# Kernel tuning notes

Measured on AMD Instinct MI355X. Metric: run time of the kernel, lower is better.

Reference implementation:

```python
import jax, jax.numpy as jnp
import numpy as np

B, P, K, F, H = 128, 200, 60, 4, 64   # events, points/event, knn k, feat dim, hidden
N = B * P


def setup_inputs() -> dict:
    key = jax.random.key(0)
    k0, k1, k2, k3 = jax.random.split(key, 4)
    x = jax.random.normal(k0, (N, F), jnp.float32)
    pos = jax.random.normal(k1, (N, 3), jnp.float32)
    batch = jnp.arange(N, dtype=jnp.int32) // P  # sorted event ids, equal-size events
    W1 = jax.random.normal(k2, (F + 3, H), jnp.float32) / np.sqrt(F + 3)
    b1 = jnp.zeros((H,), jnp.float32)
    W2 = jax.random.normal(k3, (H, H), jnp.float32) / np.sqrt(H)
    b2 = jnp.zeros((H,), jnp.float32)
    return {"x": x, "pos": pos, "batch": batch, "W1": W1, "b1": b1, "W2": W2, "b2": b2}


def _knn_edges(pos):
    """knn_graph(pos, K, batch, loop=False, flow='source_to_target').
    Equal-size events -> batched [B,P,P] pairwise distances, no cross-event edges."""
    p = pos.reshape(B, P, 3)
    d2 = jnp.sum((p[:, :, None, :] - p[:, None, :, :]) ** 2, axis=-1)  # [B,P,P]
    d2 = d2 + jnp.eye(P, dtype=d2.dtype) * 1e10                        # exclude self (loop=False)
    _, nbr = jax.lax.top_k(-d2, K)                                     # [B,P,K] local neighbor ids
    src = (nbr + (jnp.arange(B, dtype=nbr.dtype) * P)[:, None, None]).reshape(-1)  # sources j
    dst = jnp.repeat(jnp.arange(N, dtype=src.dtype), K)                             # targets i
    return jnp.stack([src, dst])  # [2, N*K]


def _local_nn(m, W1, b1, W2, b2):
    h = jax.nn.relu(m @ W1 + b1)
    return jax.nn.relu(h @ W2 + b2)


def reference(x, pos, batch, W1, b1, W2, b2):
    edge_index = _knn_edges(pos)
    src, dst = edge_index[0], edge_index[1]
    # PointConv message: net(concat[x_j, pos_j - pos_i]) on each edge
    rel = pos[src] - pos[dst]                             # [E,3]
    m = jnp.concatenate([x[src], rel], axis=-1)           # [E,F+3]
    h = _local_nn(m, W1, b1, W2, b2)                      # [E,H]
    out = h.reshape(N, K, H).max(axis=1)                  # max-aggregate per target node
    # PyG PointConv adds self-loops by default: message with rel = 0
    m_self = jnp.concatenate([x, jnp.zeros((N, 3), x.dtype)], axis=-1)
    h_self = _local_nn(m_self, W1, b1, W2, b2)            # [N,H]
    out = jnp.maximum(out, h_self)
    return (out, pos, batch, edge_index)
```

## Files before the change

kernel.cpp:

```cpp
#include <hip/hip_runtime.h>
#include <hip/hip_bf16.h>

typedef unsigned int u32;
typedef unsigned long long u64;
typedef __attribute__((ext_vector_type(8))) short bf16x8;
typedef __attribute__((ext_vector_type(4))) float f32x4;
typedef __attribute__((ext_vector_type(4))) u32 u32x4;
typedef __attribute__((ext_vector_type(2))) u32 u32x2;

#define NB 128
#define PP 200
#define KK 60
#define NN (NB*PP)
#define HH 64
#define TW 2
#define NWV 4
#define TB (TW*NWV)
#define BPE (PP/TB)
#define NTHREADS (NWV*64)

#define OUT_OFF   0
#define POS_OFF   (NN*HH)
#define BATCH_OFF (POS_OFF + NN*3)
#define ESRC_OFF  (BATCH_OFF + NN)
#define EDST_OFF  (ESRC_OFF + NN*KK)

static __device__ __forceinline__ u32 packtr(float a, float b) {
    return __builtin_amdgcn_perm(__float_as_uint(b), __float_as_uint(a), 0x07060302u);
}
static __device__ __forceinline__ u32 prefix_lt(u64 b) {
    return __builtin_amdgcn_mbcnt_hi((u32)(b >> 32),
                                     __builtin_amdgcn_mbcnt_lo((u32)b, 0));
}
static __device__ __forceinline__ float wavemax16(float v) {
    u32 x = __float_as_uint(v);
    auto p16 = __builtin_amdgcn_permlane16_swap(x, x, false, false);
    float m = fmaxf(__uint_as_float(p16[0]), __uint_as_float(p16[1]));
    u32 y = __float_as_uint(m);
    auto p32 = __builtin_amdgcn_permlane32_swap(y, y, false, false);
    return fmaxf(__uint_as_float(p32[0]), __uint_as_float(p32[1]));
}

__global__ __launch_bounds__(NTHREADS) void fused_kernel(const float* __restrict__ x,
                                                    const float* __restrict__ pos,
                                                    const float* __restrict__ W1,
                                                    const float* __restrict__ b1p,
                                                    const float* __restrict__ W2,
                                                    const float* __restrict__ b2p,
                                                    float* __restrict__ out) {
    __shared__ alignas(16) u32 xsp[PP * 2];
    __shared__ alignas(16) float psl[PP * 3];
    __shared__ alignas(16) u32 jslot[NWV * TW * 64];
    __shared__ alignas(16) u32 msg[NWV * 256];
    __shared__ alignas(16) u32 pkW1[64 * 4];
    __shared__ alignas(16) u32 pkW2T[64 * 33];
    __shared__ alignas(16) float b2s[64];
    __shared__ alignas(16) u32 zrow[4];

    int tid = threadIdx.x, blk = blockIdx.x;
    int e = blk / BPE;
    int pl0b = (blk % BPE) * TB;
    int i0b  = e * PP + pl0b;

    if (tid < 3*TB) out[POS_OFF + i0b * 3 + tid] = pos[i0b * 3 + tid];
    if (tid < TB)   out[BATCH_OFF + i0b + tid] = (float)e;

    if (tid < 200) {
        f32x4 xv = ((const f32x4*)x)[e * PP + tid];
        u32x2 p; p[0] = packtr(xv[0], xv[1]); p[1] = packtr(xv[2], xv[3]);
        *(u32x2*)&xsp[tid * 2] = p;
    }
    if (tid < 150) ((f32x4*)psl)[tid] = ((const f32x4*)pos)[e * 150 + tid];
    if (tid < 4)   zrow[tid] = 0u;

    {
        int m = tid & 63, d = tid >> 6;
        float hiv = (d < 3) ? W1[(2*d + 1)*64 + m] : b1p[m];
        pkW1[m*4 + d] = packtr(W1[(2*d)*64 + m], hiv);
    }
    #pragma unroll
    for (int r = 0; r < 4; ++r) {
        int g = r * NTHREADS + tid;
        int kp = g >> 4, colq = g & 15;
        f32x4 ra = *(const f32x4*)&W2[(2*kp)    *64 + colq*4];
        f32x4 rb = *(const f32x4*)&W2[(2*kp + 1)*64 + colq*4];
        #pragma unroll
        for (int c = 0; c < 4; ++c)
            pkW2T[(colq*4 + c)*33 + kp] = packtr(ra[c], rb[c]);
    }
    if (tid < 64) b2s[tid] = b2p[tid];
    __syncthreads();

    int lane = tid & 63, wv = tid >> 6;
    int lo16 = lane & 15, hi16 = lane >> 4;
    int plW0 = pl0b + wv * TW;
    int iW0  = e * PP + plW0;

    #pragma unroll
    for (int t = 0; t < TW; ++t)
        if (lane < KK) out[EDST_OFF + (iW0 + t) * KK + lane] = (float)(iW0 + t);

    u32 key[TW][4];
    {
        float ax[TW], ay[TW], az[TW];
        #pragma unroll
        for (int t = 0; t < TW; ++t) {
            ax[t] = psl[(plW0+t)*3]; ay[t] = psl[(plW0+t)*3+1]; az[t] = psl[(plW0+t)*3+2];
        }
        #pragma unroll
        for (int q = 0; q < 4; ++q) {
            int j = lane + q * 64;
            int jc = (j < PP) ? j : 0;
            float px = psl[jc*3], py = psl[jc*3+1], pz = psl[jc*3+2];
            #pragma unroll
            for (int t = 0; t < TW; ++t) {
                float dx = px-ax[t], dy = py-ay[t], dz = pz-az[t];
                float d2 = dx*dx + dy*dy + dz*dz;
                key[t][q] = (j < PP && j != plW0 + t)
                          ? ((__float_as_uint(d2) & 0xFFFFFF00u) | (u32)j) : 0xFFFFFFFFu;
            }
        }
    }

    bf16x8 w1f[4];
    #pragma unroll
    for (int th = 0; th < 4; ++th) {
        union { u32 w[4]; bf16x8 v; } u;
        if (hi16 == 0) *(u32x4*)u.w = *(const u32x4*)&pkW1[(th * 16 + lo16) * 4];
        else { u.w[0] = u.w[1] = u.w[2] = u.w[3] = 0u; }
        w1f[th] = u.v;
    }
    bf16x8 bfr[4][2];
    #pragma unroll
    for (int t = 0; t < 4; ++t)
        #pragma unroll
        for (int s = 0; s < 2; ++s) {
            union { u32 w[4]; bf16x8 v; } u;
            int base = (t * 16 + lo16) * 33 + s * 16 + hi16 * 4;
            #pragma unroll
            for (int d = 0; d < 4; ++d) u.w[d] = pkW2T[base + d];
            bfr[t][s] = u.v;
        }
    float b2me = b2s[lane];

    u32 lo[TW], hi[TW]; int done[TW];
    #pragma unroll
    for (int t = 0; t < TW; ++t) { lo[t] = 0u; hi[t] = 0x7F800000u; done[t] = 0; }
    #pragma unroll 1
    for (int g = 0; g < 8; ++g) {
        #pragma unroll
        for (int u4 = 0; u4 < 4; ++u4) {
            #pragma unroll
            for (int t = 0; t < TW; ++t) {
                u32 m = lo[t] + ((hi[t] - lo[t]) >> 1);
                int c = __builtin_popcountll(__ballot(key[t][0] < m))
                      + __builtin_popcountll(__ballot(key[t][1] < m))
                      + __builtin_popcountll(__ballot(key[t][2] < m))
                      + __builtin_popcountll(__ballot(key[t][3] < m));
                int upd = !done[t];
                int ge  = (c >= KK);
                hi[t] = (upd & ge)  ? m : hi[t];
                lo[t] = (upd & !ge) ? m : lo[t];
                done[t] |= (c == KK) | (hi[t] - lo[t] <= 1u);
            }
        }
        int alldone = done[0];
        #pragma unroll
        for (int t = 1; t < TW; ++t) alldone &= done[t];
        if (alldone) break;
    }

    const int jsb = wv * (TW * 64);
    #pragma unroll
    for (int t = 0; t < TW; ++t) {
        if (lane >= KK) jslot[jsb + t * 64 + lane] = (u32)(plW0 + t);
        u64 m0 = __ballot(key[t][0] < hi[t]);
        u64 m1 = __ballot(key[t][1] < hi[t]);
        u64 m2 = __ballot(key[t][2] < hi[t]);
        u64 m3 = __ballot(key[t][3] < hi[t]);
        u32 s1 = (u32)__builtin_popcountll(m0);
        u32 s2 = s1 + (u32)__builtin_popcountll(m1);
        u32 s3 = s2 + (u32)__builtin_popcountll(m2);
        u32 sl[4] = { prefix_lt(m0), s1 + prefix_lt(m1),
                      s2 + prefix_lt(m2), s3 + prefix_lt(m3) };
        #pragma unroll
        for (int q = 0; q < 4; ++q)
            if (key[t][q] < hi[t]) jslot[jsb + t * 64 + (int)sl[q]] = key[t][q] & 0xFFu;
    }
    #pragma unroll
    for (int t = 0; t < TW; ++t) {
        int i = iW0 + t;
        if (lane < KK)
            out[ESRC_OFF + i * KK + lane] = (float)(e * PP + (int)jslot[jsb + t * 64 + lane]);
    }

    const int msb = wv * 256;
    const u32* mbase = (hi16 == 0) ? &msg[msb + lo16 * 4] : zrow;
    const int mstep  = (hi16 == 0) ? 64 : 0;

    for (int tl = 0; tl < TW; ++tl) {
        int i = iW0 + tl, pl = plW0 + tl;
        int jloc = (int)jslot[jsb + tl * 64 + lane];
        u32x2 xp = *(const u32x2*)&xsp[jloc * 2];
        float rx = psl[jloc*3]   - psl[pl*3];
        float ry = psl[jloc*3+1] - psl[pl*3+1];
        float rz = psl[jloc*3+2] - psl[pl*3+2];
        u32x4 mrow;
        mrow[0] = xp[0];
        mrow[1] = xp[1];
        mrow[2] = packtr(rx, ry);
        mrow[3] = packtr(rz, 1.0f);
        *(u32x4*)&msg[msb + lane * 4] = mrow;

        float rmax[4] = {-3.0e38f, -3.0e38f, -3.0e38f, -3.0e38f};
        __builtin_amdgcn_s_setprio(1);
        #pragma unroll
        for (int rt = 0; rt < 4; ++rt) {
            union { u32 w[4]; bf16x8 v; } mu;
            *(u32x4*)mu.w = *(const u32x4*)(mbase + rt * mstep);

            f32x4 c1[4];
            #pragma unroll
            for (int th = 0; th < 4; ++th)
                c1[th] = __builtin_amdgcn_mfma_f32_16x16x32_bf16(w1f[th], mu.v,
                                                                 (f32x4)0.f, 0, 0, 0);
            f32x4 acc[4];
            #pragma unroll
            for (int t = 0; t < 4; ++t) acc[t] = (f32x4)0.f;

            #pragma unroll
            for (int s = 0; s < 2; ++s) {
                u32 pe0 = packtr(fmaxf(c1[2*s][0], 0.f), fmaxf(c1[2*s][1], 0.f));
                u32 pe1 = packtr(fmaxf(c1[2*s][2], 0.f), fmaxf(c1[2*s][3], 0.f));
                u32 po0 = packtr(fmaxf(c1[2*s+1][0], 0.f), fmaxf(c1[2*s+1][1], 0.f));
                u32 po1 = packtr(fmaxf(c1[2*s+1][2], 0.f), fmaxf(c1[2*s+1][3], 0.f));
                union { u32 w[4]; bf16x8 v; } u;
                {
                    auto t0 = __builtin_amdgcn_permlane32_swap(pe0, po0, false, false);
                    auto w0 = __builtin_amdgcn_permlane16_swap(t0[0], t0[1], false, false);
                    u.w[0] = w0[0]; u.w[2] = w0[1];
                }
                {
                    auto t1 = __builtin_amdgcn_permlane32_swap(pe1, po1, false, false);
                    auto w1 = __builtin_amdgcn_permlane16_swap(t1[0], t1[1], false, false);
                    u.w[1] = w1[0]; u.w[3] = w1[1];
                }
                #pragma unroll
                for (int t = 0; t < 4; ++t)
                    acc[t] = __builtin_amdgcn_mfma_f32_16x16x32_bf16(u.v, bfr[t][s],
                                                                     acc[t], 0, 0, 0);
            }
            #pragma unroll
            for (int t = 0; t < 4; ++t) {
                rmax[t] = fmaxf(fmaxf(acc[t][0], acc[t][1]), rmax[t]);
                rmax[t] = fmaxf(fmaxf(acc[t][2], acc[t][3]), rmax[t]);
            }
        }
        __builtin_amdgcn_s_setprio(0);
        #pragma unroll
        for (int t = 0; t < 4; ++t) rmax[t] = wavemax16(rmax[t]);
        float sel = rmax[0];
        sel = (hi16 == 1) ? rmax[1] : sel;
        sel = (hi16 == 2) ? rmax[2] : sel;
        sel = (hi16 == 3) ? rmax[3] : sel;
        out[OUT_OFF + i * 64 + lane] = fmaxf(sel + b2me, 0.f);
    }
}

extern "C" void kernel_launch(void* const* d_in, const int* in_sizes, int n_in,
                              void* d_out, int out_size, void* d_ws, size_t ws_size,
                              hipStream_t stream) {
    const float* x     = (const float*)d_in[0];
    const float* pos   = (const float*)d_in[1];
    const float* W1    = (const float*)d_in[3];
    const float* b1    = (const float*)d_in[4];
    const float* W2    = (const float*)d_in[5];
    const float* b2    = (const float*)d_in[6];
    float* out = (float*)d_out;
    (void)d_ws; (void)ws_size; (void)in_sizes; (void)n_in; (void)out_size;

    fused_kernel<<<dim3(NN / TB), dim3(NTHREADS), 0, stream>>>(x, pos, W1, b1, W2, b2, out);
}
```

Measured before the change: 113.7 us.

## Tighten kNN bisection bounds and pass MFMA message rows via permlane

The threshold bisection for the k-th nearest distance now starts from the wave-wide min and max key, found with shuffle and permlane reductions, rather than the full float range. Tuples that have converged skip further ballot rounds. Message rows for the first-layer MFMA are no longer staged through LDS; each rt slice is built in registers with permlane16/32 swaps, which removes the msg and zrow shared buffers and their store/load round trip. The cost is two extra wave reductions per tuple and cross-lane permutes in the inner loop, and the upper lanes' zero-padding semantics now differ, so the B-operand layout may not match the previous zero-filled rows.

```diff
diff --git a/kernel.cpp b/kernel.cpp
--- a/kernel.cpp
+++ b/kernel.cpp
@@ -40,6 +40,26 @@
     auto p32 = __builtin_amdgcn_permlane32_swap(y, y, false, false);
     return fmaxf(__uint_as_float(p32[0]), __uint_as_float(p32[1]));
 }
+static __device__ __forceinline__ u32 wredmin_u32(u32 v) {
+    v = min(v, (u32)__shfl_xor((int)v, 1, 64));
+    v = min(v, (u32)__shfl_xor((int)v, 2, 64));
+    v = min(v, (u32)__shfl_xor((int)v, 4, 64));
+    v = min(v, (u32)__shfl_xor((int)v, 8, 64));
+    auto p16 = __builtin_amdgcn_permlane16_swap(v, v, false, false);
+    v = min((u32)p16[0], (u32)p16[1]);
+    auto p32 = __builtin_amdgcn_permlane32_swap(v, v, false, false);
+    return min((u32)p32[0], (u32)p32[1]);
+}
+static __device__ __forceinline__ u32 wredmax_u32(u32 v) {
+    v = max(v, (u32)__shfl_xor((int)v, 1, 64));
+    v = max(v, (u32)__shfl_xor((int)v, 2, 64));
+    v = max(v, (u32)__shfl_xor((int)v, 4, 64));
+    v = max(v, (u32)__shfl_xor((int)v, 8, 64));
+    auto p16 = __builtin_amdgcn_permlane16_swap(v, v, false, false);
+    v = max((u32)p16[0], (u32)p16[1]);
+    auto p32 = __builtin_amdgcn_permlane32_swap(v, v, false, false);
+    return max((u32)p32[0], (u32)p32[1]);
+}
 
 __global__ __launch_bounds__(NTHREADS) void fused_kernel(const float* __restrict__ x,
                                                     const float* __restrict__ pos,
@@ -51,11 +71,9 @@
     __shared__ alignas(16) u32 xsp[PP * 2];
     __shared__ alignas(16) float psl[PP * 3];
     __shared__ alignas(16) u32 jslot[NWV * TW * 64];
-    __shared__ alignas(16) u32 msg[NWV * 256];
     __shared__ alignas(16) u32 pkW1[64 * 4];
     __shared__ alignas(16) u32 pkW2T[64 * 33];
     __shared__ alignas(16) float b2s[64];
-    __shared__ alignas(16) u32 zrow[4];
 
     int tid = threadIdx.x, blk = blockIdx.x;
     int e = blk / BPE;
@@ -71,7 +89,6 @@
         *(u32x2*)&xsp[tid * 2] = p;
     }
     if (tid < 150) ((f32x4*)psl)[tid] = ((const f32x4*)pos)[e * 150 + tid];
-    if (tid < 4)   zrow[tid] = 0u;
 
     {
         int m = tid & 63, d = tid >> 6;
@@ -145,23 +162,26 @@
 
     u32 lo[TW], hi[TW]; int done[TW];
     #pragma unroll
-    for (int t = 0; t < TW; ++t) { lo[t] = 0u; hi[t] = 0x7F800000u; done[t] = 0; }
+    for (int t = 0; t < TW; ++t) {
+        u32 mn = min(min(key[t][0], key[t][1]), min(key[t][2], key[t][3]));
+        u32 mx = max(max(key[t][0] + 1u, key[t][1] + 1u),
+                     max(key[t][2] + 1u, key[t][3] + 1u));
+        lo[t] = wredmin_u32(mn);
+        hi[t] = wredmax_u32(mx);
+        done[t] = 0;
+    }
     #pragma unroll 1
-    for (int g = 0; g < 8; ++g) {
-        #pragma unroll
-        for (int u4 = 0; u4 < 4; ++u4) {
-            #pragma unroll
-            for (int t = 0; t < TW; ++t) {
+    for (int it = 0; it < 32; ++it) {
+        #pragma unroll
+        for (int t = 0; t < TW; ++t) {
+            if (!done[t]) {
                 u32 m = lo[t] + ((hi[t] - lo[t]) >> 1);
                 int c = __builtin_popcountll(__ballot(key[t][0] < m))
                       + __builtin_popcountll(__ballot(key[t][1] < m))
                       + __builtin_popcountll(__ballot(key[t][2] < m))
                       + __builtin_popcountll(__ballot(key[t][3] < m));
-                int upd = !done[t];
-                int ge  = (c >= KK);
-                hi[t] = (upd & ge)  ? m : hi[t];
-                lo[t] = (upd & !ge) ? m : lo[t];
-                done[t] |= (c == KK) | (hi[t] - lo[t] <= 1u);
+                if (c >= KK) hi[t] = m; else lo[t] = m;
+                done[t] = (c == KK) | (hi[t] - lo[t] <= 1u);
             }
         }
         int alldone = done[0];
@@ -194,10 +214,6 @@
             out[ESRC_OFF + i * KK + lane] = (float)(e * PP + (int)jslot[jsb + t * 64 + lane]);
     }
 
-    const int msb = wv * 256;
-    const u32* mbase = (hi16 == 0) ? &msg[msb + lo16 * 4] : zrow;
-    const int mstep  = (hi16 == 0) ? 64 : 0;
-
     for (int tl = 0; tl < TW; ++tl) {
         int i = iW0 + tl, pl = plW0 + tl;
         int jloc = (int)jslot[jsb + tl * 64 + lane];
@@ -205,19 +221,33 @@
         float rx = psl[jloc*3]   - psl[pl*3];
         float ry = psl[jloc*3+1] - psl[pl*3+1];
         float rz = psl[jloc*3+2] - psl[pl*3+2];
-        u32x4 mrow;
-        mrow[0] = xp[0];
-        mrow[1] = xp[1];
-        mrow[2] = packtr(rx, ry);
-        mrow[3] = packtr(rz, 1.0f);
-        *(u32x4*)&msg[msb + lane * 4] = mrow;
+        u32 mr[4];
+        mr[0] = xp[0];
+        mr[1] = xp[1];
+        mr[2] = packtr(rx, ry);
+        mr[3] = packtr(rz, 1.0f);
 
         float rmax[4] = {-3.0e38f, -3.0e38f, -3.0e38f, -3.0e38f};
         __builtin_amdgcn_s_setprio(1);
         #pragma unroll
         for (int rt = 0; rt < 4; ++rt) {
             union { u32 w[4]; bf16x8 v; } mu;
-            *(u32x4*)mu.w = *(const u32x4*)(mbase + rt * mstep);
+            #pragma unroll
+            for (int d = 0; d < 4; ++d) {
+                if (rt == 0) {
+                    mu.w[d] = mr[d];
+                } else if (rt == 1) {
+                    auto p = __builtin_amdgcn_permlane16_swap(mr[d], mr[d], false, false);
+                    mu.w[d] = p[1];
+                } else if (rt == 2) {
+                    auto p = __builtin_amdgcn_permlane32_swap(mr[d], mr[d], false, false);
+                    mu.w[d] = p[1];
+                } else {
+                    auto p = __builtin_amdgcn_permlane32_swap(mr[d], mr[d], false, false);
+                    auto q = __builtin_amdgcn_permlane16_swap(p[1], p[1], false, false);
+                    mu.w[d] = q[1];
+                }
+            }
 
             f32x4 c1[4];
             #pragma unroll
```

New measurement: 120.1 us. 1.06x slower.

## Process two point tiles per block to amortize per-block setup

Applied to the files above, without the earlier changes.

Each block now handles up to two 8-point tiles of an event instead of one, so the event's x/pos staging and the W1/W2 bf16 packing into shared memory are done once per two tiles. The grid shrinks from 3200 to 1664 blocks, and the last block of each event handles a single tile. Pos output is now copied from shared memory. The bisection loop is also restructured so that only unfinished targets are updated under a branch, with a cap of 40 iterations. This trades fewer, longer blocks for less redundant setup and may reduce latency hiding or create tail imbalance.

```diff
diff --git a/kernel.cpp b/kernel.cpp
--- a/kernel.cpp
+++ b/kernel.cpp
@@ -16,7 +16,9 @@
 #define TW 2
 #define NWV 4
 #define TB (TW*NWV)
-#define BPE (PP/TB)
+#define NTILE 25
+#define TPB 2
+#define BPE 13
 #define NTHREADS (NWV*64)
 
 #define OUT_OFF   0
@@ -58,12 +60,9 @@
     __shared__ alignas(16) u32 zrow[4];
 
     int tid = threadIdx.x, blk = blockIdx.x;
-    int e = blk / BPE;
-    int pl0b = (blk % BPE) * TB;
-    int i0b  = e * PP + pl0b;
-
-    if (tid < 3*TB) out[POS_OFF + i0b * 3 + tid] = pos[i0b * 3 + tid];
-    if (tid < TB)   out[BATCH_OFF + i0b + tid] = (float)e;
+    int e   = blk / BPE;
+    int tb0 = (blk % BPE) * TPB;
+    int ntile = (tb0 + 1 < NTILE) ? TPB : 1;
 
     if (tid < 200) {
         f32x4 xv = ((const f32x4*)x)[e * PP + tid];
@@ -93,177 +92,182 @@
 
     int lane = tid & 63, wv = tid >> 6;
     int lo16 = lane & 15, hi16 = lane >> 4;
-    int plW0 = pl0b + wv * TW;
-    int iW0  = e * PP + plW0;
-
-    #pragma unroll
-    for (int t = 0; t < TW; ++t)
-        if (lane < KK) out[EDST_OFF + (iW0 + t) * KK + lane] = (float)(iW0 + t);
-
-    u32 key[TW][4];
-    {
-        float ax[TW], ay[TW], az[TW];
-        #pragma unroll
-        for (int t = 0; t < TW; ++t) {
-            ax[t] = psl[(plW0+t)*3]; ay[t] = psl[(plW0+t)*3+1]; az[t] = psl[(plW0+t)*3+2];
-        }
-        #pragma unroll
-        for (int q = 0; q < 4; ++q) {
-            int j = lane + q * 64;
-            int jc = (j < PP) ? j : 0;
-            float px = psl[jc*3], py = psl[jc*3+1], pz = psl[jc*3+2];
-            #pragma unroll
-            for (int t = 0; t < TW; ++t) {
-                float dx = px-ax[t], dy = py-ay[t], dz = pz-az[t];
-                float d2 = dx*dx + dy*dy + dz*dz;
-                key[t][q] = (j < PP && j != plW0 + t)
-                          ? ((__float_as_uint(d2) & 0xFFFFFF00u) | (u32)j) : 0xFFFFFFFFu;
-            }
-        }
-    }
-
-    bf16x8 w1f[4];
-    #pragma unroll
-    for (int th = 0; th < 4; ++th) {
-        union { u32 w[4]; bf16x8 v; } u;
-        if (hi16 == 0) *(u32x4*)u.w = *(const u32x4*)&pkW1[(th * 16 + lo16) * 4];
-        else { u.w[0] = u.w[1] = u.w[2] = u.w[3] = 0u; }
-        w1f[th] = u.v;
-    }
-    bf16x8 bfr[4][2];
-    #pragma unroll
-    for (int t = 0; t < 4; ++t)
-        #pragma unroll
-        for (int s = 0; s < 2; ++s) {
-            union { u32 w[4]; bf16x8 v; } u;
-            int base = (t * 16 + lo16) * 33 + s * 16 + hi16 * 4;
-            #pragma unroll
-            for (int d = 0; d < 4; ++d) u.w[d] = pkW2T[base + d];
-            bfr[t][s] = u.v;
-        }
     float b2me = b2s[lane];
-
-    u32 lo[TW], hi[TW]; int done[TW];
-    #pragma unroll
-    for (int t = 0; t < TW; ++t) { lo[t] = 0u; hi[t] = 0x7F800000u; done[t] = 0; }
-    #pragma unroll 1
-    for (int g = 0; g < 8; ++g) {
-        #pragma unroll
-        for (int u4 = 0; u4 < 4; ++u4) {
-            #pragma unroll
-            for (int t = 0; t < TW; ++t) {
-                u32 m = lo[t] + ((hi[t] - lo[t]) >> 1);
-                int c = __builtin_popcountll(__ballot(key[t][0] < m))
-                      + __builtin_popcountll(__ballot(key[t][1] < m))
-                      + __builtin_popcountll(__ballot(key[t][2] < m))
-                      + __builtin_popcountll(__ballot(key[t][3] < m));
-                int upd = !done[t];
-                int ge  = (c >= KK);
-                hi[t] = (upd & ge)  ? m : hi[t];
-                lo[t] = (upd & !ge) ? m : lo[t];
-                done[t] |= (c == KK) | (hi[t] - lo[t] <= 1u);
-            }
-        }
-        int alldone = done[0];
-        #pragma unroll
-        for (int t = 1; t < TW; ++t) alldone &= done[t];
-        if (alldone) break;
-    }
-
     const int jsb = wv * (TW * 64);
-    #pragma unroll
-    for (int t = 0; t < TW; ++t) {
-        if (lane >= KK) jslot[jsb + t * 64 + lane] = (u32)(plW0 + t);
-        u64 m0 = __ballot(key[t][0] < hi[t]);
-        u64 m1 = __ballot(key[t][1] < hi[t]);
-        u64 m2 = __ballot(key[t][2] < hi[t]);
-        u64 m3 = __ballot(key[t][3] < hi[t]);
-        u32 s1 = (u32)__builtin_popcountll(m0);
-        u32 s2 = s1 + (u32)__builtin_popcountll(m1);
-        u32 s3 = s2 + (u32)__builtin_popcountll(m2);
-        u32 sl[4] = { prefix_lt(m0), s1 + prefix_lt(m1),
-                      s2 + prefix_lt(m2), s3 + prefix_lt(m3) };
-        #pragma unroll
-        for (int q = 0; q < 4; ++q)
-            if (key[t][q] < hi[t]) jslot[jsb + t * 64 + (int)sl[q]] = key[t][q] & 0xFFu;
-    }
-    #pragma unroll
-    for (int t = 0; t < TW; ++t) {
-        int i = iW0 + t;
-        if (lane < KK)
-            out[ESRC_OFF + i * KK + lane] = (float)(e * PP + (int)jslot[jsb + t * 64 + lane]);
-    }
-
     const int msb = wv * 256;
     const u32* mbase = (hi16 == 0) ? &msg[msb + lo16 * 4] : zrow;
     const int mstep  = (hi16 == 0) ? 64 : 0;
 
-    for (int tl = 0; tl < TW; ++tl) {
-        int i = iW0 + tl, pl = plW0 + tl;
-        int jloc = (int)jslot[jsb + tl * 64 + lane];
-        u32x2 xp = *(const u32x2*)&xsp[jloc * 2];
-        float rx = psl[jloc*3]   - psl[pl*3];
-        float ry = psl[jloc*3+1] - psl[pl*3+1];
-        float rz = psl[jloc*3+2] - psl[pl*3+2];
-        u32x4 mrow;
-        mrow[0] = xp[0];
-        mrow[1] = xp[1];
-        mrow[2] = packtr(rx, ry);
-        mrow[3] = packtr(rz, 1.0f);
-        *(u32x4*)&msg[msb + lane * 4] = mrow;
-
-        float rmax[4] = {-3.0e38f, -3.0e38f, -3.0e38f, -3.0e38f};
-        __builtin_amdgcn_s_setprio(1);
-        #pragma unroll
-        for (int rt = 0; rt < 4; ++rt) {
-            union { u32 w[4]; bf16x8 v; } mu;
-            *(u32x4*)mu.w = *(const u32x4*)(mbase + rt * mstep);
-
-            f32x4 c1[4];
-            #pragma unroll
-            for (int th = 0; th < 4; ++th)
-                c1[th] = __builtin_amdgcn_mfma_f32_16x16x32_bf16(w1f[th], mu.v,
-                                                                 (f32x4)0.f, 0, 0, 0);
-            f32x4 acc[4];
-            #pragma unroll
-            for (int t = 0; t < 4; ++t) acc[t] = (f32x4)0.f;
-
+    #pragma unroll 1
+    for (int ti = 0; ti < ntile; ++ti) {
+        int pl0 = (tb0 + ti) * TB;
+        int i0  = e * PP + pl0;
+
+        if (tid < 3*TB) out[POS_OFF + i0 * 3 + tid] = psl[pl0 * 3 + tid];
+        if (tid < TB)   out[BATCH_OFF + i0 + tid] = (float)e;
+
+        int plW0 = pl0 + wv * TW;
+        int iW0  = e * PP + plW0;
+
+        #pragma unroll
+        for (int t = 0; t < TW; ++t)
+            if (lane < KK) out[EDST_OFF + (iW0 + t) * KK + lane] = (float)(iW0 + t);
+
+        u32 key[TW][4];
+        {
+            float ax[TW], ay[TW], az[TW];
+            #pragma unroll
+            for (int t = 0; t < TW; ++t) {
+                ax[t] = psl[(plW0+t)*3]; ay[t] = psl[(plW0+t)*3+1]; az[t] = psl[(plW0+t)*3+2];
+            }
+            #pragma unroll
+            for (int q = 0; q < 4; ++q) {
+                int j = lane + q * 64;
+                int jc = (j < PP) ? j : 0;
+                float px = psl[jc*3], py = psl[jc*3+1], pz = psl[jc*3+2];
+                #pragma unroll
+                for (int t = 0; t < TW; ++t) {
+                    float dx = px-ax[t], dy = py-ay[t], dz = pz-az[t];
+                    float d2 = dx*dx + dy*dy + dz*dz;
+                    key[t][q] = (j < PP && j != plW0 + t)
+                              ? ((__float_as_uint(d2) & 0xFFFFFF00u) | (u32)j) : 0xFFFFFFFFu;
+                }
+            }
+        }
+
+        u32 lo[TW], hi[TW]; int done[TW];
+        #pragma unroll
+        for (int t = 0; t < TW; ++t) { lo[t] = 0u; hi[t] = 0x7F800000u; done[t] = 0; }
+        #pragma unroll 1
+        for (int it = 0; it < 40; ++it) {
+            #pragma unroll
+            for (int t = 0; t < TW; ++t) {
+                if (!done[t]) {
+                    u32 m = lo[t] + ((hi[t] - lo[t]) >> 1);
+                    int c = __builtin_popcountll(__ballot(key[t][0] < m))
+                          + __builtin_popcountll(__ballot(key[t][1] < m))
+                          + __builtin_popcountll(__ballot(key[t][2] < m))
+                          + __builtin_popcountll(__ballot(key[t][3] < m));
+                    if (c >= KK) hi[t] = m; else lo[t] = m;
+                    done[t] = (c == KK) | (hi[t] - lo[t] <= 1u);
+                }
+            }
+            int alldone = done[0];
+            #pragma unroll
+            for (int t = 1; t < TW; ++t) alldone &= done[t];
+            if (alldone) break;
+        }
+
+        #pragma unroll
+        for (int t = 0; t < TW; ++t) {
+            if (lane >= KK) jslot[jsb + t * 64 + lane] = (u32)(plW0 + t);
+            u64 m0 = __ballot(key[t][0] < hi[t]);
+            u64 m1 = __ballot(key[t][1] < hi[t]);
+            u64 m2 = __ballot(key[t][2] < hi[t]);
+            u64 m3 = __ballot(key[t][3] < hi[t]);
+            u32 s1 = (u32)__builtin_popcountll(m0);
+            u32 s2 = s1 + (u32)__builtin_popcountll(m1);
+            u32 s3 = s2 + (u32)__builtin_popcountll(m2);
+            u32 sl[4] = { prefix_lt(m0), s1 + prefix_lt(m1),
+                          s2 + prefix_lt(m2), s3 + prefix_lt(m3) };
+            #pragma unroll
+            for (int q = 0; q < 4; ++q)
+                if (key[t][q] < hi[t]) jslot[jsb + t * 64 + (int)sl[q]] = key[t][q] & 0xFFu;
+        }
+        #pragma unroll
+        for (int t = 0; t < TW; ++t) {
+            int i = iW0 + t;
+            if (lane < KK)
+                out[ESRC_OFF + i * KK + lane] = (float)(e * PP + (int)jslot[jsb + t * 64 + lane]);
+        }
+
+        bf16x8 w1f[4];
+        #pragma unroll
+        for (int th = 0; th < 4; ++th) {
+            union { u32 w[4]; bf16x8 v; } u;
+            if (hi16 == 0) *(u32x4*)u.w = *(const u32x4*)&pkW1[(th * 16 + lo16) * 4];
+            else { u.w[0] = u.w[1] = u.w[2] = u.w[3] = 0u; }
+            w1f[th] = u.v;
+        }
+        bf16x8 bfr[4][2];
+        #pragma unroll
+        for (int t = 0; t < 4; ++t)
             #pragma unroll
             for (int s = 0; s < 2; ++s) {
-                u32 pe0 = packtr(fmaxf(c1[2*s][0], 0.f), fmaxf(c1[2*s][1], 0.f));
-                u32 pe1 = packtr(fmaxf(c1[2*s][2], 0.f), fmaxf(c1[2*s][3], 0.f));
-                u32 po0 = packtr(fmaxf(c1[2*s+1][0], 0.f), fmaxf(c1[2*s+1][1], 0.f));
-                u32 po1 = packtr(fmaxf(c1[2*s+1][2], 0.f), fmaxf(c1[2*s+1][3], 0.f));
                 union { u32 w[4]; bf16x8 v; } u;
-                {
-                    auto t0 = __builtin_amdgcn_permlane32_swap(pe0, po0, false, false);
-                    auto w0 = __builtin_amdgcn_permlane16_swap(t0[0], t0[1], false, false);
-                    u.w[0] = w0[0]; u.w[2] = w0[1];
-                }
-                {
-                    auto t1 = __builtin_amdgcn_permlane32_swap(pe1, po1, false, false);
-                    auto w1 = __builtin_amdgcn_permlane16_swap(t1[0], t1[1], false, false);
-                    u.w[1] = w1[0]; u.w[3] = w1[1];
-                }
-                #pragma unroll
-                for (int t = 0; t < 4; ++t)
-                    acc[t] = __builtin_amdgcn_mfma_f32_16x16x32_bf16(u.v, bfr[t][s],
-                                                                     acc[t], 0, 0, 0);
-            }
-            #pragma unroll
-            for (int t = 0; t < 4; ++t) {
-                rmax[t] = fmaxf(fmaxf(acc[t][0], acc[t][1]), rmax[t]);
-                rmax[t] = fmaxf(fmaxf(acc[t][2], acc[t][3]), rmax[t]);
-            }
-        }
-        __builtin_amdgcn_s_setprio(0);
-        #pragma unroll
-        for (int t = 0; t < 4; ++t) rmax[t] = wavemax16(rmax[t]);
-        float sel = rmax[0];
-        sel = (hi16 == 1) ? rmax[1] : sel;
-        sel = (hi16 == 2) ? rmax[2] : sel;
-        sel = (hi16 == 3) ? rmax[3] : sel;
-        out[OUT_OFF + i * 64 + lane] = fmaxf(sel + b2me, 0.f);
+                int base = (t * 16 + lo16) * 33 + s * 16 + hi16 * 4;
+                #pragma unroll
+                for (int d = 0; d < 4; ++d) u.w[d] = pkW2T[base + d];
+                bfr[t][s] = u.v;
+            }
+
+        for (int tl = 0; tl < TW; ++tl) {
+            int i = iW0 + tl, pl = plW0 + tl;
+            int jloc = (int)jslot[jsb + tl * 64 + lane];
+            u32x2 xp = *(const u32x2*)&xsp[jloc * 2];
+            float rx = psl[jloc*3]   - psl[pl*3];
+            float ry = psl[jloc*3+1] - psl[pl*3+1];
+            float rz = psl[jloc*3+2] - psl[pl*3+2];
+            u32x4 mrow;
+            mrow[0] = xp[0];
+            mrow[1] = xp[1];
+            mrow[2] = packtr(rx, ry);
+            mrow[3] = packtr(rz, 1.0f);
+            *(u32x4*)&msg[msb + lane * 4] = mrow;
+
+            float rmax[4] = {-3.0e38f, -3.0e38f, -3.0e38f, -3.0e38f};
+            __builtin_amdgcn_s_setprio(1);
+            #pragma unroll
+            for (int rt = 0; rt < 4; ++rt) {
+                union { u32 w[4]; bf16x8 v; } mu;
+                *(u32x4*)mu.w = *(const u32x4*)(mbase + rt * mstep);
+
+                f32x4 c1[4];
+                #pragma unroll
+                for (int th = 0; th < 4; ++th)
+                    c1[th] = __builtin_amdgcn_mfma_f32_16x16x32_bf16(w1f[th], mu.v,
+                                                                     (f32x4)0.f, 0, 0, 0);
+                f32x4 acc[4];
+                #pragma unroll
+                for (int t = 0; t < 4; ++t) acc[t] = (f32x4)0.f;
+
+                #pragma unroll
+                for (int s = 0; s < 2; ++s) {
+                    u32 pe0 = packtr(fmaxf(c1[2*s][0], 0.f), fmaxf(c1[2*s][1], 0.f));
+                    u32 pe1 = packtr(fmaxf(c1[2*s][2], 0.f), fmaxf(c1[2*s][3], 0.f));
+                    u32 po0 = packtr(fmaxf(c1[2*s+1][0], 0.f), fmaxf(c1[2*s+1][1], 0.f));
+                    u32 po1 = packtr(fmaxf(c1[2*s+1][2], 0.f), fmaxf(c1[2*s+1][3], 0.f));
+                    union { u32 w[4]; bf16x8 v; } u;
+                    {
+                        auto t0 = __builtin_amdgcn_permlane32_swap(pe0, po0, false, false);
+                        auto w0 = __builtin_amdgcn_permlane16_swap(t0[0], t0[1], false, false);
+                        u.w[0] = w0[0]; u.w[2] = w0[1];
+                    }
+                    {
+                        auto t1 = __builtin_amdgcn_permlane32_swap(pe1, po1, false, false);
+                        auto w1 = __builtin_amdgcn_permlane16_swap(t1[0], t1[1], false, false);
+                        u.w[1] = w1[0]; u.w[3] = w1[1];
+                    }
+                    #pragma unroll
+                    for (int t = 0; t < 4; ++t)
+                        acc[t] = __builtin_amdgcn_mfma_f32_16x16x32_bf16(u.v, bfr[t][s],
+                                                                         acc[t], 0, 0, 0);
+                }
+                #pragma unroll
+                for (int t = 0; t < 4; ++t) {
+                    rmax[t] = fmaxf(fmaxf(acc[t][0], acc[t][1]), rmax[t]);
+                    rmax[t] = fmaxf(fmaxf(acc[t][2], acc[t][3]), rmax[t]);
+                }
+            }
+            __builtin_amdgcn_s_setprio(0);
+            #pragma unroll
+            for (int t = 0; t < 4; ++t) rmax[t] = wavemax16(rmax[t]);
+            float sel = rmax[0];
+            sel = (hi16 == 1) ? rmax[1] : sel;
+            sel = (hi16 == 2) ? rmax[2] : sel;
+            sel = (hi16 == 3) ? rmax[3] : sel;
+            out[OUT_OFF + i * 64 + lane] = fmaxf(sel + b2me, 0.f);
+        }
     }
 }
 
@@ -279,5 +283,5 @@
     float* out = (float*)d_out;
     (void)d_ws; (void)ws_size; (void)in_sizes; (void)n_in; (void)out_size;
 
-    fused_kernel<<<dim3(NN / TB), dim3(NTHREADS), 0, stream>>>(x, pos, W1, b1, W2, b2, out);
-}
+    fused_kernel<<<dim3(NB * BPE), dim3(NTHREADS), 0, stream>>>(x, pos, W1, b1, W2, b2, out);
+}
```

After: 117.4 us. +3.2%, slower.

## Process one target point per wavefront instead of two, doubling block count

Applied to the files above, without the earlier changes.

Removes the TW=2 per-wave batching, so each wave handles a single target point. Blocks now cover 4 points instead of 8, which doubles the grid to 6400 blocks. The bisection loop becomes a simple early-exit loop per wave. The cost is more blocks, each repeating the per-block setup work: loading x and pos for the whole event and packing W1 and W2 into LDS. The pos output copy now reads from LDS instead of global memory.

```diff
diff --git a/kernel.cpp b/kernel.cpp
--- a/kernel.cpp
+++ b/kernel.cpp
@@ -13,9 +13,8 @@
 #define KK 60
 #define NN (NB*PP)
 #define HH 64
-#define TW 2
 #define NWV 4
-#define TB (TW*NWV)
+#define TB NWV
 #define BPE (PP/TB)
 #define NTHREADS (NWV*64)
 
@@ -50,7 +49,7 @@
                                                     float* __restrict__ out) {
     __shared__ alignas(16) u32 xsp[PP * 2];
     __shared__ alignas(16) float psl[PP * 3];
-    __shared__ alignas(16) u32 jslot[NWV * TW * 64];
+    __shared__ alignas(16) u32 jslot[NWV * 64];
     __shared__ alignas(16) u32 msg[NWV * 256];
     __shared__ alignas(16) u32 pkW1[64 * 4];
     __shared__ alignas(16) u32 pkW2T[64 * 33];
@@ -58,12 +57,9 @@
     __shared__ alignas(16) u32 zrow[4];
 
     int tid = threadIdx.x, blk = blockIdx.x;
-    int e = blk / BPE;
+    int e    = blk / BPE;
     int pl0b = (blk % BPE) * TB;
     int i0b  = e * PP + pl0b;
-
-    if (tid < 3*TB) out[POS_OFF + i0b * 3 + tid] = pos[i0b * 3 + tid];
-    if (tid < TB)   out[BATCH_OFF + i0b + tid] = (float)e;
 
     if (tid < 200) {
         f32x4 xv = ((const f32x4*)x)[e * PP + tid];
@@ -93,32 +89,32 @@
 
     int lane = tid & 63, wv = tid >> 6;
     int lo16 = lane & 15, hi16 = lane >> 4;
-    int plW0 = pl0b + wv * TW;
-    int iW0  = e * PP + plW0;
-
-    #pragma unroll
-    for (int t = 0; t < TW; ++t)
-        if (lane < KK) out[EDST_OFF + (iW0 + t) * KK + lane] = (float)(iW0 + t);
-
-    u32 key[TW][4];
-    {
-        float ax[TW], ay[TW], az[TW];
-        #pragma unroll
-        for (int t = 0; t < TW; ++t) {
-            ax[t] = psl[(plW0+t)*3]; ay[t] = psl[(plW0+t)*3+1]; az[t] = psl[(plW0+t)*3+2];
-        }
+    float b2me = b2s[lane];
+    const int jsb = wv * 64;
+    const int msb = wv * 256;
+    const u32* mbase = (hi16 == 0) ? &msg[msb + lo16 * 4] : zrow;
+    const int mstep  = (hi16 == 0) ? 64 : 0;
+
+    if (tid < 3*TB) out[POS_OFF + i0b * 3 + tid] = psl[pl0b * 3 + tid];
+    if (tid < TB)   out[BATCH_OFF + i0b + tid] = (float)e;
+
+    int pl = pl0b + wv;
+    int i  = e * PP + pl;
+
+    if (lane < KK) out[EDST_OFF + i * KK + lane] = (float)i;
+
+    u32 key[4];
+    {
+        float ax = psl[pl*3], ay = psl[pl*3+1], az = psl[pl*3+2];
         #pragma unroll
         for (int q = 0; q < 4; ++q) {
             int j = lane + q * 64;
             int jc = (j < PP) ? j : 0;
             float px = psl[jc*3], py = psl[jc*3+1], pz = psl[jc*3+2];
-            #pragma unroll
-            for (int t = 0; t < TW; ++t) {
-                float dx = px-ax[t], dy = py-ay[t], dz = pz-az[t];
-                float d2 = dx*dx + dy*dy + dz*dz;
-                key[t][q] = (j < PP && j != plW0 + t)
-                          ? ((__float_as_uint(d2) & 0xFFFFFF00u) | (u32)j) : 0xFFFFFFFFu;
-            }
+            float dx = px-ax, dy = py-ay, dz = pz-az;
+            float d2 = dx*dx + dy*dy + dz*dz;
+            key[q] = (j < PP && j != pl)
+                   ? ((__float_as_uint(d2) & 0xFFFFFF00u) | (u32)j) : 0xFFFFFFFFu;
         }
     }
 
@@ -141,43 +137,25 @@
             for (int d = 0; d < 4; ++d) u.w[d] = pkW2T[base + d];
             bfr[t][s] = u.v;
         }
-    float b2me = b2s[lane];
-
-    u32 lo[TW], hi[TW]; int done[TW];
-    #pragma unroll
-    for (int t = 0; t < TW; ++t) { lo[t] = 0u; hi[t] = 0x7F800000u; done[t] = 0; }
+
+    u32 lo = 0u, hi = 0x7F800000u;
     #pragma unroll 1
-    for (int g = 0; g < 8; ++g) {
-        #pragma unroll
-        for (int u4 = 0; u4 < 4; ++u4) {
-            #pragma unroll
-            for (int t = 0; t < TW; ++t) {
-                u32 m = lo[t] + ((hi[t] - lo[t]) >> 1);
-                int c = __builtin_popcountll(__ballot(key[t][0] < m))
-                      + __builtin_popcountll(__ballot(key[t][1] < m))
-                      + __builtin_popcountll(__ballot(key[t][2] < m))
-                      + __builtin_popcountll(__ballot(key[t][3] < m));
-                int upd = !done[t];
-                int ge  = (c >= KK);
-                hi[t] = (upd & ge)  ? m : hi[t];
-                lo[t] = (upd & !ge) ? m : lo[t];
-                done[t] |= (c == KK) | (hi[t] - lo[t] <= 1u);
-            }
-        }
-        int alldone = done[0];
-        #pragma unroll
-        for (int t = 1; t < TW; ++t) alldone &= done[t];
-        if (alldone) break;
-    }
-
-    const int jsb = wv * (TW * 64);
-    #pragma unroll
-    for (int t = 0; t < TW; ++t) {
-        if (lane >= KK) jslot[jsb + t * 64 + lane] = (u32)(plW0 + t);
-        u64 m0 = __ballot(key[t][0] < hi[t]);
-        u64 m1 = __ballot(key[t][1] < hi[t]);
-        u64 m2 = __ballot(key[t][2] < hi[t]);
-        u64 m3 = __ballot(key[t][3] < hi[t]);
+    for (int it = 0; it < 40; ++it) {
+        u32 m = lo + ((hi - lo) >> 1);
+        int c = __builtin_popcountll(__ballot(key[0] < m))
+              + __builtin_popcountll(__ballot(key[1] < m))
+              + __builtin_popcountll(__ballot(key[2] < m))
+              + __builtin_popcountll(__ballot(key[3] < m));
+        if (c >= KK) hi = m; else lo = m;
+        if ((c == KK) | (hi - lo <= 1u)) break;
+    }
+
+    if (lane >= KK) jslot[jsb + lane] = (u32)pl;
+    {
+        u64 m0 = __ballot(key[0] < hi);
+        u64 m1 = __ballot(key[1] < hi);
+        u64 m2 = __ballot(key[2] < hi);
+        u64 m3 = __ballot(key[3] < hi);
         u32 s1 = (u32)__builtin_popcountll(m0);
         u32 s2 = s1 + (u32)__builtin_popcountll(m1);
         u32 s3 = s2 + (u32)__builtin_popcountll(m2);
@@ -185,22 +163,13 @@
                       s2 + prefix_lt(m2), s3 + prefix_lt(m3) };
         #pragma unroll
         for (int q = 0; q < 4; ++q)
-            if (key[t][q] < hi[t]) jslot[jsb + t * 64 + (int)sl[q]] = key[t][q] & 0xFFu;
-    }
-    #pragma unroll
-    for (int t = 0; t < TW; ++t) {
-        int i = iW0 + t;
-        if (lane < KK)
-            out[ESRC_OFF + i * KK + lane] = (float)(e * PP + (int)jslot[jsb + t * 64 + lane]);
-    }
-
-    const int msb = wv * 256;
-    const u32* mbase = (hi16 == 0) ? &msg[msb + lo16 * 4] : zrow;
-    const int mstep  = (hi16 == 0) ? 64 : 0;
-
-    for (int tl = 0; tl < TW; ++tl) {
-        int i = iW0 + tl, pl = plW0 + tl;
-        int jloc = (int)jslot[jsb + tl * 64 + lane];
+            if (key[q] < hi) jslot[jsb + (int)sl[q]] = key[q] & 0xFFu;
+    }
+    if (lane < KK)
+        out[ESRC_OFF + i * KK + lane] = (float)(e * PP + (int)jslot[jsb + lane]);
+
+    {
+        int jloc = (int)jslot[jsb + lane];
         u32x2 xp = *(const u32x2*)&xsp[jloc * 2];
         float rx = psl[jloc*3]   - psl[pl*3];
         float ry = psl[jloc*3+1] - psl[pl*3+1];
```

Measured after the change: 110.7 us. 1.03x faster.
